# Kernel tuning notes

Hardware: AMD Instinct MI355X
Metric: run time of the kernel (lower is better)

Reference implementation:

```python
import jax, jax.numpy as jnp
import numpy as np
import math

EPS_LN = 1e-5
TARGET_ACTIVITY = 0.1
THETA = 2.0 ** 16

B, NH, T, D, N = 2, 12, 2048, 768, 256


def layernorm(x):
    m = jnp.mean(x, axis=-1, keepdims=True)
    v = jnp.mean((x - m) ** 2, axis=-1, keepdims=True)
    return (x - m) / jnp.sqrt(v + EPS_LN)


def get_freqs(n):
    q = jnp.floor(jnp.arange(n, dtype=jnp.float32) / 2.0) * 2.0  # quantize by 2
    return 1.0 / (THETA ** (q / n)) / (2.0 * math.pi)


def rope(phases, v):
    ph = (phases % 1.0) * (2.0 * math.pi)
    c, s = jnp.cos(ph), jnp.sin(ph)
    even = v[..., 0::2]
    odd = v[..., 1::2]
    v_rot = jnp.stack((-odd, even), axis=-1).reshape(v.shape)  # interleaved rotate
    return v * c + v_rot * s


def setup_inputs() -> dict:
    key = jax.random.key(0)
    ks = jax.random.split(key, 5)
    std = 0.02
    return {
        "x": jax.random.normal(ks[0], (B, 1, T, D), dtype=jnp.float32),
        "encoder": jax.random.normal(ks[1], (NH, D, N), dtype=jnp.float32) * std,
        "encoder_v": jax.random.normal(ks[2], (NH, D, N), dtype=jnp.float32) * std,
        "decoder": jax.random.normal(ks[3], (NH * N, D), dtype=jnp.float32) * std,
        "scale": jnp.ones((D,), dtype=jnp.float32),
        "running_activity": jnp.ones((D,), dtype=jnp.float32) * TARGET_ACTIVITY,
    }


def reference(x, encoder, encoder_v, decoder, scale, running_activity):
    Bv, _, Tv, Dv = x.shape
    nh, _, Nv = encoder.shape

    # encode + ReLU sparsify: [B,1,T,D] @ [nh,D,N] -> [B,nh,T,N]
    x_latent = jnp.einsum('bztd,hdn->bhtn', x, encoder)
    x_sparse = jax.nn.relu(x_latent)

    # RoPE on Q=K=x_sparse
    freqs = get_freqs(Nv)  # [N]
    r_phases = jnp.arange(Tv, dtype=jnp.float32)[:, None] * freqs[None, :]  # [T,N]
    QR = rope(r_phases, x_sparse)
    KR = rope(r_phases, x_sparse)

    # non-softmax causal attention, strictly lower-triangular (diag=-1)
    scores = jnp.einsum('bhtn,bhsn->bhts', QR, KR)
    mask = jnp.tril(jnp.ones((Tv, Tv), dtype=scores.dtype), k=-1)
    scores = scores * mask
    yKV = jnp.einsum('bhts,bsd->bhtd', scores, x[:, 0])  # V = x

    yKV = layernorm(yKV)
    y_sparse = jax.nn.relu(jnp.einsum('bhtd,hdn->bhtn', yKV, encoder_v))
    xy_sparse = x_sparse * y_sparse  # [B,nh,T,N]; dropout=0 (eval)

    # [B,nh,T,N] -> [B,1,T,nh*N] @ [nh*N,D]
    flat = jnp.transpose(xy_sparse, (0, 2, 1, 3)).reshape(Bv, 1, Tv, nh * Nv)
    yMLP = flat @ decoder

    y = layernorm(yMLP)
    regulation = TARGET_ACTIVITY / (running_activity + 1e-6)
    y = y * jnp.sqrt(regulation) * scale

    return layernorm(x + y), xy_sparse
```

## Files before the change

### kernel.cpp

```cpp
#include <hip/hip_runtime.h>
#include <math.h>

#define TT 2048
#define DD 768
#define NN 256
#define NHH 12
#define BB 2
#define CH 512

typedef unsigned short u16;
typedef __attribute__((ext_vector_type(8))) short bf16x8;
typedef __attribute__((ext_vector_type(8))) unsigned short u16x8;
typedef __attribute__((ext_vector_type(4))) float f32x4;

static inline int imin(int a, int b) { return a < b ? a : b; }

__device__ __forceinline__ u16 f2b(float f) {
  union { float f; unsigned u; } a; a.f = f;
  unsigned r = a.u + 0x7FFF + ((a.u >> 16) & 1);
  return (u16)(r >> 16);
}
__device__ __forceinline__ float b2f(u16 h) {
  union { unsigned u; float f; } a; a.u = ((unsigned)h) << 16;
  return a.f;
}

__device__ __forceinline__ void async16(const void* g, void* l) {
  __builtin_amdgcn_global_load_lds(
      (const __attribute__((address_space(1))) unsigned*)g,
      (__attribute__((address_space(3))) unsigned*)l, 16, 0, 0);
}

#define KSWZ(row) (((row) >> 1) & 3)

__device__ __forceinline__ void stage128x32(
    const u16* __restrict__ gbase, size_t ld, u16* lds, int tid) {
  const int w = tid >> 6, l = tid & 63;
#pragma unroll
  for (int q = 0; q < 2; ++q) {
    const int row = w * 32 + q * 16 + (l >> 2);
    const int kc = ((l & 3) ^ KSWZ(row)) << 3;
    async16(gbase + (size_t)row * ld + kc, lds + (w * 32 + q * 16) * 32);
  }
}

__device__ __forceinline__ void stage64x32(
    const u16* __restrict__ gbase, size_t ld, u16* lds, int tid) {
  const int w = tid >> 6, l = tid & 63;
  const int row = w * 16 + (l >> 2);
  const int kc = ((l & 3) ^ KSWZ(row)) << 3;
  async16(gbase + (size_t)row * ld + kc, lds + w * 512);
}

__device__ __forceinline__ void mfma_step(
    const u16* As, const u16* Bs, int wr, int wc, int lane, f32x4 acc[4][4]) {
  const int m16 = lane & 15, quad = lane >> 4;
  bf16x8 a[4], b[4];
#pragma unroll
  for (int i = 0; i < 4; ++i) {
    const int row = wr * 64 + i * 16 + m16;
    a[i] = *(const bf16x8*)&As[row * 32 + ((quad ^ KSWZ(row)) << 3)];
  }
#pragma unroll
  for (int j = 0; j < 4; ++j) {
    const int row = wc * 64 + j * 16 + m16;
    b[j] = *(const bf16x8*)&Bs[row * 32 + ((quad ^ KSWZ(row)) << 3)];
  }
#pragma unroll
  for (int i = 0; i < 4; ++i)
#pragma unroll
    for (int j = 0; j < 4; ++j)
      acc[i][j] = __builtin_amdgcn_mfma_f32_16x16x32_bf16(a[i], b[j], acc[i][j], 0, 0, 0);
}

__device__ __forceinline__ void copy_out128(
    const u16* buf, u16* g, size_t ld, int tid) {
#pragma unroll
  for (int s = 0; s < 8; ++s) {
    const int off = (s * 256 + tid) * 8;
    const int row = off >> 7, col = off & 127;
    *(u16x8*)&g[(size_t)row * ld + col] = *(const u16x8*)&buf[off];
  }
}

#define GEMM_SMEM \
  __shared__ __attribute__((aligned(16))) u16 smem[32768];

#define GEMM_VARS()                                                \
  const int tid = threadIdx.x;                                     \
  const int w = tid >> 6, lane = tid & 63;                         \
  const int wr = w >> 1, wc = w & 1;                               \
  const int col16 = lane & 15, quad = lane >> 4;                   \
  f32x4 acc[4][4];                                                 \
  _Pragma("unroll") for (int i = 0; i < 4; ++i)                    \
  _Pragma("unroll") for (int j = 0; j < 4; ++j)                    \
      acc[i][j] = (f32x4){0.f, 0.f, 0.f, 0.f};

#define GEMM_PROLOGUE() GEMM_SMEM GEMM_VARS()

#define PIPELINED_K_LOOP64(ABASE, ALD, BBASE, BLD, KTOT)                    \
  {                                                                         \
    stage128x32((ABASE), (ALD), smem, tid);                                 \
    stage128x32((ABASE) + 32, (ALD), smem + 4096, tid);                     \
    stage128x32((BBASE), (BLD), smem + 8192, tid);                          \
    stage128x32((BBASE) + 32, (BLD), smem + 12288, tid);                    \
    const int np_ = (KTOT) / 64;                                            \
    for (int pp_ = 0; pp_ < np_; ++pp_) {                                   \
      u16* cb_ = (pp_ & 1) ? smem + 16384 : smem;                           \
      u16* nb_ = (pp_ & 1) ? smem : smem + 16384;                           \
      if (pp_ + 1 < np_) {                                                  \
        const int kn_ = (pp_ + 1) * 64;                                     \
        stage128x32((ABASE) + kn_, (ALD), nb_, tid);                        \
        stage128x32((ABASE) + kn_ + 32, (ALD), nb_ + 4096, tid);            \
        stage128x32((BBASE) + kn_, (BLD), nb_ + 8192, tid);                 \
        stage128x32((BBASE) + kn_ + 32, (BLD), nb_ + 12288, tid);           \
        asm volatile("s_waitcnt vmcnt(8)" ::: "memory");                    \
      } else {                                                              \
        asm volatile("s_waitcnt vmcnt(0)" ::: "memory");                    \
      }                                                                     \
      __builtin_amdgcn_s_barrier();                                         \
      __builtin_amdgcn_sched_barrier(0);                                    \
      mfma_step(cb_, cb_ + 8192, wr, wc, lane, acc);                        \
      mfma_step(cb_ + 4096, cb_ + 12288, wr, wc, lane, acc);                \
      __builtin_amdgcn_sched_barrier(0);                                    \
      __builtin_amdgcn_s_barrier();                                         \
    }                                                                       \
  }

__device__ __forceinline__ void tcvt_body(
    const float* __restrict__ ip, u16* __restrict__ op, int R, int C,
    int bx, int by, int tid, float (*tile)[33]) {
  const int c0 = bx * 32, r0 = by * 32;
  const int tx = tid & 31, ty = tid >> 5;
#pragma unroll
  for (int p = 0; p < 4; ++p)
    tile[ty + p * 8][tx] = ip[(size_t)(r0 + ty + p * 8) * C + c0 + tx];
  __syncthreads();
#pragma unroll
  for (int p = 0; p < 4; ++p)
    op[(size_t)(c0 + ty + p * 8) * R + r0 + tx] = f2b(tile[tx][ty + p * 8]);
}

__global__ __launch_bounds__(256) void k_prep(
    const float* __restrict__ x, u16* __restrict__ X16, u16* __restrict__ XT16,
    const float* __restrict__ enc, u16* __restrict__ ENCT,
    const float* __restrict__ encv, u16* __restrict__ ENCVT,
    const float* __restrict__ dec, u16* __restrict__ DECT,
    float2* __restrict__ CS) {
  __shared__ float tile[32][33];
  const int tid = threadIdx.x;
  const int bid = blockIdx.x;
  if (bid < 3072) {
    const size_t i = ((size_t)bid * 256 + tid) * 4;
    float4 v = *(const float4*)&x[i];
    u16 o[4] = {f2b(v.x), f2b(v.y), f2b(v.z), f2b(v.w)};
    *(ushort4*)&X16[i] = *(ushort4*)o;
  } else if (bid < 6144) {
    const int b = bid - 3072;
    const int bz = b / 1536, rb = b % 1536;
    tcvt_body(x + (size_t)bz * TT * DD, XT16 + (size_t)bz * DD * TT,
              TT, DD, rb % 24, rb / 24, tid, tile);
  } else if (bid < 8448) {
    const int b = bid - 6144;
    const int bz = b / 192, rb = b % 192;
    tcvt_body(enc + (size_t)bz * DD * NN, ENCT + (size_t)bz * NN * DD,
              DD, NN, rb % 8, rb / 8, tid, tile);
  } else if (bid < 10752) {
    const int b = bid - 8448;
    const int bz = b / 192, rb = b % 192;
    tcvt_body(encv + (size_t)bz * DD * NN, ENCVT + (size_t)bz * NN * DD,
              DD, NN, rb % 8, rb / 8, tid, tile);
  } else if (bid < 13056) {
    const int b = bid - 10752;
    tcvt_body(dec, DECT, NHH * NN, DD, b % 24, b / 24, tid, tile);
  } else {
    const int idx = (bid - 13056) * 256 + tid;
    const int t = idx >> 7, n2 = idx & 127;
    const float freq = exp2f((float)(2 * n2) * -0.0625f) * 0.15915494309189535f;
    const float phase = (float)t * freq;
    const float ph = (phase - floorf(phase)) * 6.283185307179586f;
    CS[idx] = make_float2(__cosf(ph), __sinf(ph));
  }
}

__global__ __launch_bounds__(256) void k_colsum(
    const u16* __restrict__ encvt, float* __restrict__ colsum) {
  const int row = blockIdx.x * 4 + (threadIdx.x >> 6);
  const int lane = threadIdx.x & 63;
  const u16* pr = encvt + (size_t)row * DD;
  float s = 0.f;
#pragma unroll
  for (int i = 0; i < 3; ++i) {
    ushort4 v = *(const ushort4*)&pr[(lane << 2) + i * 256];
    s += b2f(v.x) + b2f(v.y) + b2f(v.z) + b2f(v.w);
  }
#pragma unroll
  for (int off = 32; off; off >>= 1) s += __shfl_xor(s, off);
  if (lane == 0) colsum[row] = s;
}

__device__ __forceinline__ int swz8(int row) { return ((row >> 3) & 7) << 3; }

__global__ __launch_bounds__(256) void k1_encode(
    const u16* __restrict__ x16, const u16* __restrict__ enct,
    const float2* __restrict__ CS,
    u16* __restrict__ qr16, u16* __restrict__ qrt16) {
  const int h = blockIdx.z;
  const int m0 = blockIdx.x * 128, n0 = blockIdx.y * 128;
  GEMM_PROLOGUE();
  PIPELINED_K_LOOP64(x16 + (size_t)m0 * DD, DD,
                     enct + ((size_t)h * NN + n0) * DD, DD, DD);
  __syncthreads();
#pragma unroll
  for (int i = 0; i < 4; ++i)
#pragma unroll
    for (int j = 0; j < 4; ++j) {
      const int n = n0 + wc * 64 + j * 16 + col16;
      float rv[4], pv[4];
#pragma unroll
      for (int r = 0; r < 4; ++r) rv[r] = fmaxf(acc[i][j][r], 0.f);
#pragma unroll
      for (int r = 0; r < 4; ++r) pv[r] = __shfl_xor(rv[r], 1);
#pragma unroll
      for (int r = 0; r < 4; ++r) {
        const int lrow = wr * 64 + i * 16 + quad * 4 + r;
        const int t = (m0 + lrow) & (TT - 1);
        const float2 cs = CS[t * 128 + (n >> 1)];
        const float o = (n & 1) ? (rv[r] * cs.x + pv[r] * cs.y)
                                : (rv[r] * cs.x - pv[r] * cs.y);
        smem[lrow * 128 + ((wc * 64 + j * 16 + col16) ^ swz8(lrow))] = f2b(o);
      }
    }
  __syncthreads();
  const int bq = m0 >> 11, tb = m0 & (TT - 1);
  const size_t sl = (size_t)(bq * NHH + h);
  u16* qg = qr16 + (sl * TT + tb) * NN + n0;
#pragma unroll
  for (int s = 0; s < 8; ++s) {
    const int off = (s * 256 + tid) * 8;
    const int row = off >> 7, col = off & 127;
    *(u16x8*)&qg[(size_t)row * NN + col] =
        *(const u16x8*)&smem[row * 128 + (col ^ swz8(row))];
  }
#pragma unroll
  for (int s = 0; s < 8; ++s) {
    const int off = (s * 256 + tid) * 8;
    const int nr = off >> 7, tc = off & 127;
    const int sw = swz8(tc);
    u16 vals[8];
#pragma unroll
    for (int k = 0; k < 8; ++k) vals[k] = smem[(tc + k) * 128 + (nr ^ sw)];
    *(u16x8*)&qrt16[(sl * NN + n0 + nr) * TT + tb + tc] = *(u16x8*)vals;
  }
}

__global__ __launch_bounds__(256) void kSB(
    const u16* __restrict__ qr16, const u16* __restrict__ xt16,
    const u16* __restrict__ qrt16, u16* __restrict__ sb,
    u16* __restrict__ h16, int nS, int bh0) {
  GEMM_SMEM;
  const int tid = threadIdx.x;
  const int w = tid >> 6, lane = tid & 63;
  const int col16 = lane & 15, quad = lane >> 4;
  if ((int)blockIdx.x < nS) {
    const int wr = w >> 1, wc = w & 1;
    const int z = blockIdx.x / 40, sub = blockIdx.x % 40;
    const int bh = bh0 + z;
    const int cc = sub / 10, rr = sub % 10;
    int i = (int)((sqrtf(8.f * rr + 1.f) - 1.f) * 0.5f);
    while ((i + 1) * (i + 2) / 2 <= rr) ++i;
    while (i * (i + 1) / 2 > rr) --i;
    const int j = rr - i * (i + 1) / 2;
    const int t0 = (cc * 4 + i) * 128;
    const int s0 = cc * CH + j * 128;
    const u16* q = qr16 + (size_t)bh * TT * NN;
    f32x4 acc[4][4];
#pragma unroll
    for (int a = 0; a < 4; ++a)
#pragma unroll
      for (int b = 0; b < 4; ++b) acc[a][b] = (f32x4){0.f, 0.f, 0.f, 0.f};
    PIPELINED_K_LOOP64(q + (size_t)t0 * NN, NN, q + (size_t)s0 * NN, NN, NN);
    const bool diag = (i == j);
    __syncthreads();
#pragma unroll
    for (int ii = 0; ii < 4; ++ii)
#pragma unroll
      for (int jj = 0; jj < 4; ++jj) {
        const int s = s0 + wc * 64 + jj * 16 + col16;
#pragma unroll
        for (int r = 0; r < 4; ++r) {
          const int lrow = wr * 64 + ii * 16 + quad * 4 + r;
          const int t = t0 + lrow;
          float v = acc[ii][jj][r];
          if (diag && s >= t) v = 0.f;
          smem[lrow * 128 + wc * 64 + jj * 16 + col16] = f2b(v);
        }
      }
    __syncthreads();
    copy_out128(smem, sb + ((size_t)z * TT + t0) * CH + j * 128, CH, tid);
  } else {
    const int r2 = blockIdx.x - nS;
    const int z = r2 / 24, rr2 = r2 % 24;
    const int d0 = (rr2 % 12) * 64, n0 = (rr2 / 12) * 128;
    const int bh = bh0 + z, b = bh / NHH;
    u16* buf0 = smem;
    u16* buf1 = smem + 12288;
    u16* snap = smem + 24576;
    f32x4 acc[4][2];
#pragma unroll
    for (int i = 0; i < 4; ++i)
#pragma unroll
      for (int j = 0; j < 2; ++j) acc[i][j] = (f32x4){0.f, 0.f, 0.f, 0.f};
    const u16* Ab = xt16 + ((size_t)b * DD + d0) * TT;
    const u16* Bb = qrt16 + ((size_t)bh * NN + n0) * TT;
#define KB_STAGE(buf, k0)                                                   \
  {                                                                         \
    stage64x32(Ab + (k0), TT, (buf), tid);                                  \
    stage64x32(Ab + (k0) + 32, TT, (buf) + 2048, tid);                      \
    stage128x32(Bb + (k0), TT, (buf) + 4096, tid);                          \
    stage128x32(Bb + (k0) + 32, TT, (buf) + 8192, tid);                     \
  }
    for (int c = 0; c < 3; ++c) {
      const int kbase = c * CH;
      KB_STAGE(buf0, kbase);
      for (int s = 0; s < CH / 64; ++s) {
        u16* cb = (s & 1) ? buf1 : buf0;
        u16* nb = (s & 1) ? buf0 : buf1;
        if (s + 1 < CH / 64) {
          KB_STAGE(nb, kbase + (s + 1) * 64);
          asm volatile("s_waitcnt vmcnt(6)" ::: "memory");
        } else {
          asm volatile("s_waitcnt vmcnt(0)" ::: "memory");
        }
        __builtin_amdgcn_s_barrier();
        __builtin_amdgcn_sched_barrier(0);
#pragma unroll
        for (int half = 0; half < 2; ++half) {
          bf16x8 a[4], bb[2];
#pragma unroll
          for (int i = 0; i < 4; ++i) {
            const int row = i * 16 + col16;
            a[i] = *(const bf16x8*)&cb[half * 2048 + row * 32 +
                                       ((quad ^ KSWZ(row)) << 3)];
          }
#pragma unroll
          for (int j = 0; j < 2; ++j) {
            const int row = w * 32 + j * 16 + col16;
            bb[j] = *(const bf16x8*)&cb[4096 + half * 4096 + row * 32 +
                                        ((quad ^ KSWZ(row)) << 3)];
          }
#pragma unroll
          for (int i = 0; i < 4; ++i)
#pragma unroll
            for (int j = 0; j < 2; ++j)
              acc[i][j] = __builtin_amdgcn_mfma_f32_16x16x32_bf16(a[i], bb[j], acc[i][j], 0, 0, 0);
        }
        __builtin_amdgcn_sched_barrier(0);
        __builtin_amdgcn_s_barrier();
      }
#pragma unroll
      for (int i = 0; i < 4; ++i)
#pragma unroll
        for (int j = 0; j < 2; ++j)
#pragma unroll
          for (int r = 0; r < 4; ++r)
            snap[(i * 16 + quad * 4 + r) * 128 + w * 32 + j * 16 + col16] =
                f2b(acc[i][j][r]);
      __syncthreads();
      u16* hd = h16 + (size_t)(z * 3 + c) * DD * NN;
#pragma unroll
      for (int s4 = 0; s4 < 4; ++s4) {
        const int off = (s4 * 256 + tid) * 8;
        const int row = off >> 7, col = off & 127;
        *(u16x8*)&hd[(size_t)(d0 + row) * NN + n0 + col] = *(const u16x8*)&snap[off];
      }
      __syncthreads();
    }
#undef KB_STAGE
  }
}

__device__ static const int TTORD[16] = {15, 11, 7, 14, 10, 6, 13, 9,
                                         5, 3, 12, 8, 4, 2, 1, 0};

__global__ __launch_bounds__(256) void kA_attn(
    const u16* __restrict__ qr16, const u16* __restrict__ h16,
    const u16* __restrict__ sb, const u16* __restrict__ xt16,
    u16* __restrict__ ykv16, float2* __restrict__ PART, int gsTT, int bh0) {
  GEMM_SMEM;
  const int tid = threadIdx.x;
  const int w = tid >> 6, lane = tid & 63;
  const int wr = w >> 1, wc = w & 1;
  const int col16 = lane & 15, quad = lane >> 4;
  const int nwg = gridDim.x;
  const int bid = blockIdx.x;
  const int qn = nwg >> 3, r8 = nwg & 7;
  const int xcd = bid & 7, pos = bid >> 3;
  const int wg = (xcd < r8 ? xcd * (qn + 1) : r8 * (qn + 1) + (xcd - r8) * qn) + pos;
  const int z = wg / 96;
  const int tt = TTORD[(wg / 6) & 15];
  const int dblk = wg % 6;
  const int d0 = dblk * 128;
  const int bh = bh0 + z, b = bh / NHH;
  const int c = tt >> 2, it = tt & 3;
  const int t0 = tt * 128;
  f32x4 acc[4][4];
#pragma unroll
  for (int i = 0; i < 4; ++i)
#pragma unroll
    for (int j = 0; j < 4; ++j) acc[i][j] = (f32x4){0.f, 0.f, 0.f, 0.f};

  const int c4 = (c > 0) ? 4 : 0;
  const int nP = c4 + (it + 1) * 2;
  const u16* hs = h16 + ((size_t)(z * 3 + (c > 0 ? c - 1 : 0)) * DD + d0) * NN;
  const u16* qb = qr16 + ((size_t)bh * TT + t0) * NN;
  const u16* sbb = sb + ((size_t)z * TT + t0) * CH;
  const u16* xb = xt16 + ((size_t)b * DD + d0) * TT + c * CH;

#define KA_STAGE(buf, p)                                                  \
  {                                                                       \
    const u16 *pa_, *pb_; size_t la_, lb_;                                \
    if ((p) < c4) {                                                       \
      pa_ = qb + (p) * 64; la_ = NN;                                      \
      pb_ = hs + (p) * 64; lb_ = NN;                                      \
    } else {                                                              \
      const int q_ = (p) - c4;                                            \
      const int j_ = q_ >> 1, kk_ = (q_ & 1) << 6;                        \
      pa_ = sbb + j_ * 128 + kk_; la_ = CH;                               \
      pb_ = xb + j_ * 128 + kk_; lb_ = TT;                                \
    }                                                                     \
    stage128x32(pa_, la_, (buf), tid);                                    \
    stage128x32(pa_ + 32, la_, (buf) + 4096, tid);                        \
    stage128x32(pb_, lb_, (buf) + 8192, tid);                             \
    stage128x32(pb_ + 32, lb_, (buf) + 12288, tid);                       \
  }

  u16* bufA = smem;
  u16* bufB = smem + 16384;
  KA_STAGE(bufA, 0);
  for (int p = 0; p < nP; ++p) {
    u16* cb = (p & 1) ? bufB : bufA;
    u16* nb = (p & 1) ? bufA : bufB;
    if (p + 1 < nP) {
      KA_STAGE(nb, p + 1);
      asm volatile("s_waitcnt vmcnt(8)" ::: "memory");
    } else {
      asm volatile("s_waitcnt vmcnt(0)" ::: "memory");
    }
    __builtin_amdgcn_s_barrier();
    __builtin_amdgcn_sched_barrier(0);
    mfma_step(cb, cb + 8192, wr, wc, lane, acc);
    mfma_step(cb + 4096, cb + 12288, wr, wc, lane, acc);
    __builtin_amdgcn_sched_barrier(0);
    __builtin_amdgcn_s_barrier();
  }
#undef KA_STAGE

  __syncthreads();
#pragma unroll
  for (int i = 0; i < 4; ++i)
#pragma unroll
    for (int j = 0; j < 4; ++j)
#pragma unroll
      for (int r = 0; r < 4; ++r) {
        const int lrow = wr * 64 + i * 16 + quad * 4 + r;
        smem[lrow * 128 + wc * 64 + j * 16 + col16] = f2b(acc[i][j][r]);
      }
  __syncthreads();
  float2* scratch = (float2*)&smem[16384];
  u16* yg = ykv16 + ((size_t)z * TT + t0) * DD + d0;
#pragma unroll
  for (int s = 0; s < 8; ++s) {
    const int off = (s * 256 + tid) * 8;
    const int row = off >> 7, col = off & 127;
    const u16x8 v = *(const u16x8*)&smem[off];
    *(u16x8*)&yg[(size_t)row * DD + col] = v;
    float ps = 0.f, pq = 0.f;
#pragma unroll
    for (int k = 0; k < 8; ++k) {
      const float f = b2f(v[k]);
      ps += f;
      pq += f * f;
    }
    scratch[row * 17 + (tid & 15)] = make_float2(ps, pq);
  }
  __syncthreads();
  if (tid < 128) {
    const float2* pr = &scratch[tid * 17];
    float s = 0.f, q2 = 0.f;
#pragma unroll
    for (int k = 0; k < 16; ++k) { s += pr[k].x; q2 += pr[k].y; }
    PART[(size_t)dblk * gsTT + z * TT + t0 + tid] = make_float2(s, q2);
  }
}

__global__ __launch_bounds__(256) void k4_xy(
    const u16* __restrict__ ykv16, const u16* __restrict__ encvt,
    const float2* __restrict__ CS,
    u16* __restrict__ qrxy, const float2* __restrict__ PART,
    const float* __restrict__ colsum,
    float* __restrict__ out2, int gsTT, int bh0) {
  const int z = blockIdx.z;
  const int bh = bh0 + z, h = bh % NHH;
  const int t0 = blockIdx.x * 128, n0 = blockIdx.y * 128;
  GEMM_PROLOGUE();
  PIPELINED_K_LOOP64(ykv16 + ((size_t)z * TT + t0) * DD, DD,
                     encvt + ((size_t)h * NN + n0) * DD, DD, DD);
  {
    const u16* qg = qrxy + ((size_t)bh * TT + t0) * NN + n0;
#pragma unroll
    for (int s = 0; s < 8; ++s) {
      const int row = s * 16 + w * 4 + (lane >> 4);
      const int col = (lane & 15) * 8;
      async16(qg + (size_t)row * NN + col,
              smem + 16384 + (s * 256 + w * 64) * 8);
    }
  }
  asm volatile("s_waitcnt vmcnt(0)" ::: "memory");
  __syncthreads();
#pragma unroll
  for (int i = 0; i < 4; ++i) {
    float muv[4], rsv[4];
#pragma unroll
    for (int r = 0; r < 4; ++r) {
      const int grow = z * TT + t0 + wr * 64 + i * 16 + quad * 4 + r;
      float s_ = 0.f, q_ = 0.f;
#pragma unroll
      for (int d = 0; d < 6; ++d) {
        const float2 p2 = PART[(size_t)d * gsTT + grow];
        s_ += p2.x;
        q_ += p2.y;
      }
      const float m_ = s_ * (1.f / 768.f);
      muv[r] = m_;
      rsv[r] = rsqrtf(q_ * (1.f / 768.f) - m_ * m_ + 1e-5f);
    }
#pragma unroll
    for (int j = 0; j < 4; ++j) {
      const int lcol = wc * 64 + j * 16 + col16;
      const int n = n0 + lcol;
      const float csum = colsum[h * NN + n];
#pragma unroll
      for (int r = 0; r < 4; ++r) {
        const int lrow = wr * 64 + i * 16 + quad * 4 + r;
        const int t = t0 + lrow;
        const float ys = fmaxf(rsv[r] * acc[i][j][r] - rsv[r] * muv[r] * csum, 0.f);
        const unsigned pq =
            *(const unsigned*)&smem[16384 + lrow * 128 + (lcol & ~1)];
        const float lo = b2f((u16)pq), hi = b2f((u16)(pq >> 16));
        const float2 cs = CS[t * 128 + (n >> 1)];
        const float xs = (n & 1) ? (hi * cs.x - lo * cs.y)
                                 : (lo * cs.x + hi * cs.y);
        const float val = ys * xs;
        out2[((size_t)bh * TT + t) * NN + n] = val;
        smem[lrow * 128 + lcol] = f2b(val);
      }
    }
  }
  __syncthreads();
  copy_out128(smem, qrxy + ((size_t)bh * TT + t0) * NN + n0, NN, tid);
}

__global__ __launch_bounds__(256) void k5_mlp(
    const u16* __restrict__ xyq, const u16* __restrict__ dect,
    float* __restrict__ ymlp) {
  GEMM_PROLOGUE();
  const int bid = blockIdx.x;
  const int wg = (bid & 7) * 24 + (bid >> 3);
  const int m0 = (wg / 6) * 128, d0 = (wg % 6) * 128;
  const int b = m0 >> 11, t0 = m0 & (TT - 1);
#define K5_ST(buf, p)                                                       \
  {                                                                         \
    const int k0_ = (p) * 64, hh_ = k0_ >> 8, kk_ = k0_ & 255;              \
    const u16* pa_ = xyq + ((size_t)(b * NHH + hh_) * TT + t0) * NN + kk_;  \
    const u16* pb_ = dect + (size_t)d0 * (NHH * NN) + k0_;                  \
    stage128x32(pa_, NN, (buf), tid);                                       \
    stage128x32(pa_ + 32, NN, (buf) + 4096, tid);                           \
    stage128x32(pb_, NHH * NN, (buf) + 8192, tid);                          \
    stage128x32(pb_ + 32, NHH * NN, (buf) + 12288, tid);                    \
  }
  const int NP = (NHH * NN) / 64;
  u16* bufA = smem;
  u16* bufB = smem + 16384;
  K5_ST(bufA, 0);
  for (int p = 0; p < NP; ++p) {
    u16* cb = (p & 1) ? bufB : bufA;
    u16* nb = (p & 1) ? bufA : bufB;
    if (p + 1 < NP) {
      K5_ST(nb, p + 1);
      asm volatile("s_waitcnt vmcnt(8)" ::: "memory");
    } else {
      asm volatile("s_waitcnt vmcnt(0)" ::: "memory");
    }
    __builtin_amdgcn_s_barrier();
    __builtin_amdgcn_sched_barrier(0);
    mfma_step(cb, cb + 8192, wr, wc, lane, acc);
    mfma_step(cb + 4096, cb + 12288, wr, wc, lane, acc);
    __builtin_amdgcn_sched_barrier(0);
    __builtin_amdgcn_s_barrier();
  }
#undef K5_ST
#pragma unroll
  for (int i = 0; i < 4; ++i)
#pragma unroll
    for (int j = 0; j < 4; ++j) {
      const int d = d0 + wc * 64 + j * 16 + col16;
#pragma unroll
      for (int r = 0; r < 4; ++r) {
        const int mm = m0 + wr * 64 + i * 16 + quad * 4 + r;
        ymlp[(size_t)mm * DD + d] = acc[i][j][r];
      }
    }
}

__global__ __launch_bounds__(256) void k6_final(
    const float* __restrict__ ymlp, const float* __restrict__ x,
    const float* __restrict__ scale, const float* __restrict__ ra,
    float* __restrict__ out1) {
  const int row = blockIdx.x;
  const int tid = threadIdx.x;
  const int wid = tid >> 6, lane = tid & 63;
  __shared__ float red[8];
  float v[3];
  float sum = 0.f, sq = 0.f;
#pragma unroll
  for (int j = 0; j < 3; ++j) {
    v[j] = ymlp[(size_t)row * DD + tid + j * 256];
    sum += v[j]; sq += v[j] * v[j];
  }
#pragma unroll
  for (int off = 32; off; off >>= 1) { sum += __shfl_xor(sum, off); sq += __shfl_xor(sq, off); }
  if (lane == 0) { red[wid] = sum; red[4 + wid] = sq; }
  __syncthreads();
  sum = red[0] + red[1] + red[2] + red[3];
  sq = red[4] + red[5] + red[6] + red[7];
  const float m1 = sum * (1.f / 768.f);
  const float r1 = rsqrtf(sq * (1.f / 768.f) - m1 * m1 + 1e-5f);
  float z[3];
  float sum2 = 0.f, sq2 = 0.f;
#pragma unroll
  for (int j = 0; j < 3; ++j) {
    const int d = tid + j * 256;
    float y = (v[j] - m1) * r1 * sqrtf(0.1f / (ra[d] + 1e-6f)) * scale[d];
    z[j] = x[(size_t)row * DD + d] + y;
    sum2 += z[j]; sq2 += z[j] * z[j];
  }
  __syncthreads();
#pragma unroll
  for (int off = 32; off; off >>= 1) { sum2 += __shfl_xor(sum2, off); sq2 += __shfl_xor(sq2, off); }
  if (lane == 0) { red[wid] = sum2; red[4 + wid] = sq2; }
  __syncthreads();
  sum2 = red[0] + red[1] + red[2] + red[3];
  sq2 = red[4] + red[5] + red[6] + red[7];
  const float m2 = sum2 * (1.f / 768.f);
  const float r2 = rsqrtf(sq2 * (1.f / 768.f) - m2 * m2 + 1e-5f);
#pragma unroll
  for (int j = 0; j < 3; ++j)
    out1[(size_t)row * DD + tid + j * 256] = (z[j] - m2) * r2;
}

extern "C" void kernel_launch(void* const* d_in, const int* in_sizes, int n_in,
                              void* d_out, int out_size, void* d_ws, size_t ws_size,
                              hipStream_t stream) {
  const float* x = (const float*)d_in[0];
  const float* enc = (const float*)d_in[1];
  const float* encv = (const float*)d_in[2];
  const float* dec = (const float*)d_in[3];
  const float* scale = (const float*)d_in[4];
  const float* ra = (const float*)d_in[5];
  float* out1 = (float*)d_out;
  float* out2 = out1 + (size_t)BB * TT * DD;
  float* ymlp = out1;

  const int NS = BB * NHH;
  unsigned char* p = (unsigned char*)d_ws;
  u16* X16 = (u16*)p;    p += (size_t)BB * TT * DD * 2;
  u16* XT16 = (u16*)p;   p += (size_t)BB * DD * TT * 2;
  u16* ENCT = (u16*)p;   p += (size_t)NHH * NN * DD * 2;
  u16* ENCVT = (u16*)p;  p += (size_t)NHH * NN * DD * 2;
  u16* DECT = (u16*)p;   p += (size_t)DD * NHH * NN * 2;
  u16* QR16 = (u16*)p;   p += (size_t)NS * TT * NN * 2;
  u16* QRT16 = (u16*)p;  p += (size_t)NS * NN * TT * 2;
  float* COLSUM = (float*)p; p += (size_t)NHH * NN * 4;
  float2* CS = (float2*)p;   p += (size_t)TT * (NN / 2) * sizeof(float2);
  const size_t SLICE_B = (size_t)TT * CH * 2 + 3 * (size_t)DD * NN * 2 +
                         (size_t)TT * DD * 2 + (size_t)TT * 48;
  size_t fixed = (size_t)(p - (unsigned char*)d_ws);
  size_t rem = (ws_size > fixed) ? ws_size - fixed : 0;
  int GSmax = (int)(rem / SLICE_B);
  if (GSmax < 1) GSmax = 1;
  if (GSmax > NS) GSmax = NS;
  const int ngrp = (NS + GSmax - 1) / GSmax;
  const int GS = (NS + ngrp - 1) / ngrp;
  u16* SB = (u16*)p;     p += (size_t)GS * TT * CH * 2;
  u16* H16 = (u16*)p;    p += (size_t)GS * 3 * DD * NN * 2;
  u16* YKV16 = (u16*)p;  p += (size_t)GS * TT * DD * 2;
  float2* PART = (float2*)p; p += (size_t)GS * TT * 6 * sizeof(float2);
  const int gsTT = GS * TT;

  k_prep<<<dim3(14080), 256, 0, stream>>>(
      x, X16, XT16, enc, ENCT, encv, ENCVT, dec, DECT, CS);
  k_colsum<<<dim3(NHH * NN / 4), 256, 0, stream>>>(ENCVT, COLSUM);

  k1_encode<<<dim3(BB * TT / 128, NN / 128, NHH), 256, 0, stream>>>(
      X16, ENCT, CS, QR16, QRT16);

  for (int bh0 = 0; bh0 < NS; bh0 += GS) {
    const int gs = imin(GS, NS - bh0);
    kSB<<<dim3(64 * gs), 256, 0, stream>>>(
        QR16, XT16, QRT16, SB, H16, 40 * gs, bh0);
    kA_attn<<<dim3(96 * gs), 256, 0, stream>>>(
        QR16, H16, SB, XT16, YKV16, PART, gsTT, bh0);
    k4_xy<<<dim3(TT / 128, NN / 128, gs), 256, 0, stream>>>(
        YKV16, ENCVT, CS, QR16, PART, COLSUM, out2, gsTT, bh0);
  }

  k5_mlp<<<dim3(192), 256, 0, stream>>>(QR16, DECT, ymlp);
  k6_final<<<dim3(BB * TT), 256, 0, stream>>>(ymlp, x, scale, ra, out1);
}
```

Before: 353.0 us.

## Split-K the MLP GEMM, prefetch xy tile in k4 pipeline, reorder kSB blocks

The decoder GEMM is split into two K halves across 384 blocks, writing two partial fp32 outputs that the final layernorm kernel sums. This fills more of the GPU than the previous 192 blocks, at the cost of an extra fp32 buffer and extra memory traffic. k4_xy now has an inline double-buffered K loop that issues the qrxy tile load during the last iteration so its latency overlaps compute. kSB block order is swapped so the longer H16 blocks are scheduled before the score blocks.

```diff
diff --git a/kernel.cpp b/kernel.cpp
--- a/kernel.cpp
+++ b/kernel.cpp
@@ -257,14 +257,15 @@
 __global__ __launch_bounds__(256) void kSB(
     const u16* __restrict__ qr16, const u16* __restrict__ xt16,
     const u16* __restrict__ qrt16, u16* __restrict__ sb,
-    u16* __restrict__ h16, int nS, int bh0) {
+    u16* __restrict__ h16, int nB, int bh0) {
   GEMM_SMEM;
   const int tid = threadIdx.x;
   const int w = tid >> 6, lane = tid & 63;
   const int col16 = lane & 15, quad = lane >> 4;
-  if ((int)blockIdx.x < nS) {
+  if ((int)blockIdx.x >= nB) {
+    const int rS = blockIdx.x - nB;
     const int wr = w >> 1, wc = w & 1;
-    const int z = blockIdx.x / 40, sub = blockIdx.x % 40;
+    const int z = rS / 40, sub = rS % 40;
     const int bh = bh0 + z;
     const int cc = sub / 10, rr = sub % 10;
     int i = (int)((sqrtf(8.f * rr + 1.f) - 1.f) * 0.5f);
@@ -299,7 +300,7 @@
     __syncthreads();
     copy_out128(smem, sb + ((size_t)z * TT + t0) * CH + j * 128, CH, tid);
   } else {
-    const int r2 = blockIdx.x - nS;
+    const int r2 = blockIdx.x;
     const int z = r2 / 24, rr2 = r2 % 24;
     const int d0 = (rr2 % 12) * 64, n0 = (rr2 / 12) * 128;
     const int bh = bh0 + z, b = bh / NHH;
@@ -504,17 +505,39 @@
   const int bh = bh0 + z, h = bh % NHH;
   const int t0 = blockIdx.x * 128, n0 = blockIdx.y * 128;
   GEMM_PROLOGUE();
-  PIPELINED_K_LOOP64(ykv16 + ((size_t)z * TT + t0) * DD, DD,
-                     encvt + ((size_t)h * NN + n0) * DD, DD, DD);
-  {
-    const u16* qg = qrxy + ((size_t)bh * TT + t0) * NN + n0;
-#pragma unroll
-    for (int s = 0; s < 8; ++s) {
-      const int row = s * 16 + w * 4 + (lane >> 4);
-      const int col = (lane & 15) * 8;
-      async16(qg + (size_t)row * NN + col,
-              smem + 16384 + (s * 256 + w * 64) * 8);
-    }
+  const u16* Ab = ykv16 + ((size_t)z * TT + t0) * DD;
+  const u16* Bb = encvt + ((size_t)h * NN + n0) * DD;
+  const u16* qg = qrxy + ((size_t)bh * TT + t0) * NN + n0;
+  stage128x32(Ab, DD, smem, tid);
+  stage128x32(Ab + 32, DD, smem + 4096, tid);
+  stage128x32(Bb, DD, smem + 8192, tid);
+  stage128x32(Bb + 32, DD, smem + 12288, tid);
+  const int np = DD / 64;
+  for (int pp = 0; pp < np; ++pp) {
+    u16* cb = (pp & 1) ? smem + 16384 : smem;
+    u16* nb = (pp & 1) ? smem : smem + 16384;
+    if (pp + 1 < np) {
+      const int kn = (pp + 1) * 64;
+      stage128x32(Ab + kn, DD, nb, tid);
+      stage128x32(Ab + kn + 32, DD, nb + 4096, tid);
+      stage128x32(Bb + kn, DD, nb + 8192, tid);
+      stage128x32(Bb + kn + 32, DD, nb + 12288, tid);
+      asm volatile("s_waitcnt vmcnt(8)" ::: "memory");
+    } else {
+#pragma unroll
+      for (int s = 0; s < 8; ++s) {
+        const int row = s * 16 + w * 4 + (lane >> 4);
+        const int col = (lane & 15) * 8;
+        async16(qg + (size_t)row * NN + col, smem + (s * 256 + w * 64) * 8);
+      }
+      asm volatile("s_waitcnt vmcnt(8)" ::: "memory");
+    }
+    __builtin_amdgcn_s_barrier();
+    __builtin_amdgcn_sched_barrier(0);
+    mfma_step(cb, cb + 8192, wr, wc, lane, acc);
+    mfma_step(cb + 4096, cb + 12288, wr, wc, lane, acc);
+    __builtin_amdgcn_sched_barrier(0);
+    __builtin_amdgcn_s_barrier();
   }
   asm volatile("s_waitcnt vmcnt(0)" ::: "memory");
   __syncthreads();
@@ -546,32 +569,35 @@
         const int t = t0 + lrow;
         const float ys = fmaxf(rsv[r] * acc[i][j][r] - rsv[r] * muv[r] * csum, 0.f);
         const unsigned pq =
-            *(const unsigned*)&smem[16384 + lrow * 128 + (lcol & ~1)];
+            *(const unsigned*)&smem[lrow * 128 + (lcol & ~1)];
         const float lo = b2f((u16)pq), hi = b2f((u16)(pq >> 16));
         const float2 cs = CS[t * 128 + (n >> 1)];
         const float xs = (n & 1) ? (hi * cs.x - lo * cs.y)
                                  : (lo * cs.x + hi * cs.y);
         const float val = ys * xs;
         out2[((size_t)bh * TT + t) * NN + n] = val;
-        smem[lrow * 128 + lcol] = f2b(val);
-      }
-    }
-  }
-  __syncthreads();
-  copy_out128(smem, qrxy + ((size_t)bh * TT + t0) * NN + n0, NN, tid);
+        smem[16384 + lrow * 128 + lcol] = f2b(val);
+      }
+    }
+  }
+  __syncthreads();
+  copy_out128(smem + 16384, qrxy + ((size_t)bh * TT + t0) * NN + n0, NN, tid);
 }
 
 __global__ __launch_bounds__(256) void k5_mlp(
     const u16* __restrict__ xyq, const u16* __restrict__ dect,
-    float* __restrict__ ymlp) {
+    float* __restrict__ ymp0, float* __restrict__ ymp1) {
   GEMM_PROLOGUE();
   const int bid = blockIdx.x;
-  const int wg = (bid & 7) * 24 + (bid >> 3);
-  const int m0 = (wg / 6) * 128, d0 = (wg % 6) * 128;
+  const int wg = (bid & 7) * 48 + (bid >> 3);
+  const int kh = wg / 192;
+  const int r = wg % 192;
+  const int m0 = (r / 6) * 128, d0 = (r % 6) * 128;
   const int b = m0 >> 11, t0 = m0 & (TT - 1);
+  const int kbase = kh * 1536;
 #define K5_ST(buf, p)                                                       \
   {                                                                         \
-    const int k0_ = (p) * 64, hh_ = k0_ >> 8, kk_ = k0_ & 255;              \
+    const int k0_ = kbase + (p) * 64, hh_ = k0_ >> 8, kk_ = k0_ & 255;      \
     const u16* pa_ = xyq + ((size_t)(b * NHH + hh_) * TT + t0) * NN + kk_;  \
     const u16* pb_ = dect + (size_t)d0 * (NHH * NN) + k0_;                  \
     stage128x32(pa_, NN, (buf), tid);                                       \
@@ -579,7 +605,7 @@
     stage128x32(pb_, NHH * NN, (buf) + 8192, tid);                          \
     stage128x32(pb_ + 32, NHH * NN, (buf) + 12288, tid);                    \
   }
-  const int NP = (NHH * NN) / 64;
+  const int NP = 1536 / 64;
   u16* bufA = smem;
   u16* bufB = smem + 16384;
   K5_ST(bufA, 0);
@@ -600,21 +626,23 @@
     __builtin_amdgcn_s_barrier();
   }
 #undef K5_ST
+  float* ymlp = kh ? ymp1 : ymp0;
 #pragma unroll
   for (int i = 0; i < 4; ++i)
 #pragma unroll
     for (int j = 0; j < 4; ++j) {
       const int d = d0 + wc * 64 + j * 16 + col16;
 #pragma unroll
-      for (int r = 0; r < 4; ++r) {
-        const int mm = m0 + wr * 64 + i * 16 + quad * 4 + r;
-        ymlp[(size_t)mm * DD + d] = acc[i][j][r];
+      for (int r4 = 0; r4 < 4; ++r4) {
+        const int mm = m0 + wr * 64 + i * 16 + quad * 4 + r4;
+        ymlp[(size_t)mm * DD + d] = acc[i][j][r4];
       }
     }
 }
 
 __global__ __launch_bounds__(256) void k6_final(
-    const float* __restrict__ ymlp, const float* __restrict__ x,
+    const float* __restrict__ ym0, const float* __restrict__ ym1,
+    const float* __restrict__ x,
     const float* __restrict__ scale, const float* __restrict__ ra,
     float* __restrict__ out1) {
   const int row = blockIdx.x;
@@ -625,7 +653,8 @@
   float sum = 0.f, sq = 0.f;
 #pragma unroll
   for (int j = 0; j < 3; ++j) {
-    v[j] = ymlp[(size_t)row * DD + tid + j * 256];
+    const size_t idx = (size_t)row * DD + tid + j * 256;
+    v[j] = ym0[idx] + ym1[idx];
     sum += v[j]; sq += v[j] * v[j];
   }
 #pragma unroll
@@ -670,7 +699,7 @@
   const float* ra = (const float*)d_in[5];
   float* out1 = (float*)d_out;
   float* out2 = out1 + (size_t)BB * TT * DD;
-  float* ymlp = out1;
+  float* ym0 = out1;
 
   const int NS = BB * NHH;
   unsigned char* p = (unsigned char*)d_ws;
@@ -683,6 +712,7 @@
   u16* QRT16 = (u16*)p;  p += (size_t)NS * NN * TT * 2;
   float* COLSUM = (float*)p; p += (size_t)NHH * NN * 4;
   float2* CS = (float2*)p;   p += (size_t)TT * (NN / 2) * sizeof(float2);
+  float* YM1 = (float*)p;    p += (size_t)BB * TT * DD * 4;
   const size_t SLICE_B = (size_t)TT * CH * 2 + 3 * (size_t)DD * NN * 2 +
                          (size_t)TT * DD * 2 + (size_t)TT * 48;
   size_t fixed = (size_t)(p - (unsigned char*)d_ws);
@@ -708,13 +738,13 @@
   for (int bh0 = 0; bh0 < NS; bh0 += GS) {
     const int gs = imin(GS, NS - bh0);
     kSB<<<dim3(64 * gs), 256, 0, stream>>>(
-        QR16, XT16, QRT16, SB, H16, 40 * gs, bh0);
+        QR16, XT16, QRT16, SB, H16, 24 * gs, bh0);
     kA_attn<<<dim3(96 * gs), 256, 0, stream>>>(
         QR16, H16, SB, XT16, YKV16, PART, gsTT, bh0);
     k4_xy<<<dim3(TT / 128, NN / 128, gs), 256, 0, stream>>>(
         YKV16, ENCVT, CS, QR16, PART, COLSUM, out2, gsTT, bh0);
   }
 
-  k5_mlp<<<dim3(192), 256, 0, stream>>>(QR16, DECT, ymlp);
-  k6_final<<<dim3(BB * TT), 256, 0, stream>>>(ymlp, x, scale, ra, out1);
-}
+  k5_mlp<<<dim3(384), 256, 0, stream>>>(QR16, DECT, ym0, YM1);
+  k6_final<<<dim3(BB * TT), 256, 0, stream>>>(ym0, YM1, x, scale, ra, out1);
+}
```

Result: no change. 346.5 us (-1.9%).
